# Optimization experiments

Hardware: AMD Instinct MI355X
Metric: run time of the kernel (lower is better)

## Reference

```python
import jax, jax.numpy as jnp
import numpy as np

# Sizes from init_kwargs / input_specs
D_MODEL = 1024; D_INT = 64; KW = 32; B = 2; L = 4096
SAMPLING = np.array([5, 5, 2, 1, 1]); DILATIONS = np.array([1, 1, 2, 4, 8])
SUBHEADS = len(SAMPLING); HEADS = int(SAMPLING.sum())  # 5, 14
HEAD_OF_SUB = np.repeat(np.arange(SUBHEADS), SAMPLING)  # subhead index for each head
HEAD_DIL = np.repeat(DILATIONS, SAMPLING)                # dilation for each head


def _win_idx(dil):
    # centered dilated band, clipped at sequence edges -> [L, KW]
    offs = (np.arange(KW) - KW // 2) * dil
    return np.clip(np.arange(L)[:, None] + offs[None, :], 0, L - 1)

SUB_IDX = jnp.asarray(np.stack([_win_idx(d) for d in DILATIONS]))  # [SUBHEADS, L, KW]
HEAD_IDX = jnp.asarray(np.stack([_win_idx(d) for d in HEAD_DIL]))  # [HEADS, L, KW]


def setup_inputs() -> dict:
    rng = jax.random.key(0)
    ks = jax.random.split(rng, 9)
    n = lambda i, sh, sc=1.0: jax.random.normal(ks[i], sh, dtype=jnp.float32) * sc
    return dict(
        query=n(0, (B, L, D_MODEL)),
        key=n(1, (B, L, D_MODEL)),
        value=n(2, (B, L, D_MODEL)),
        Wq=n(3, (SUBHEADS, D_MODEL, D_INT), 0.02),
        bq=jnp.zeros((SUBHEADS, D_INT), jnp.float32),
        Wk=n(4, (SUBHEADS, D_MODEL, D_INT), 0.02),
        bk=jnp.zeros((SUBHEADS, D_INT), jnp.float32),
        Wv=n(5, (HEADS, D_MODEL, D_INT), 0.02),
        bv=jnp.zeros((HEADS, D_INT), jnp.float32),
        Ws=n(6, (HEADS, KW, KW), 0.05) + jnp.eye(KW, dtype=jnp.float32)[None],
        bs=jnp.zeros((HEADS, KW), jnp.float32),
        Wc=n(7, (HEADS * D_INT, D_MODEL), 0.02),
        bc=jnp.zeros((D_MODEL,), jnp.float32),
    )


def reference(query, key, value, Wq, bq, Wk, bk, Wv, bv, Ws, bs, Wc, bc):
    # per-subhead query/key projections: [S, B, L, Di]
    q = jnp.einsum('bld,sdi->sbli', query, Wq) + bq[:, None, None, :]
    k = jnp.einsum('bld,sdi->sbli', key, Wk) + bk[:, None, None, :]
    # per-head value projection: [H, B, L, Di]
    v = jnp.einsum('bld,hdi->hbli', value, Wv) + bv[:, None, None, :]
    # dilated banded key windows per subhead: [S, B, L, KW, Di]
    kw = jax.vmap(lambda kh, ix: kh[:, ix], in_axes=(0, 0))(k, SUB_IDX)
    # banded scores [S, B, L, KW]
    scores = jnp.einsum('sbli,sblki->sblk', q, kw) / jnp.sqrt(jnp.float32(D_INT))
    # supersample: replicate each subhead's scores to its heads -> [H, B, L, KW]
    scores_h = scores[HEAD_OF_SUB]
    # per-head positional supersampling linear on the score window
    sampled = jnp.einsum('hblk,hkm->hblm', scores_h, Ws) + bs[:, None, None, :]
    attn = jax.nn.softmax(sampled, axis=-1)
    # dilated value windows per head: [H, B, L, KW, Di]
    vw = jax.vmap(lambda vh, ix: vh[:, ix], in_axes=(0, 0))(v, HEAD_IDX)
    out = jnp.einsum('hblk,hblki->hbli', attn, vw)  # [H, B, L, Di]
    out = jnp.transpose(out, (1, 2, 0, 3)).reshape(B, L, HEADS * D_INT)
    return out @ Wc + bc  # [B, L, D_MODEL]
```

## Files before the change

### kernel.cpp

```cpp
#include <hip/hip_runtime.h>
#include <math.h>

#define D_MODEL 1024
#define D_INT   64
#define KW      32
#define L_SEQ   4096
#define SUBHEADS 5
#define HEADS   14
#define M_ROWS  8192
#define N_CAT   896
#define NQK     320

typedef unsigned short us;
typedef unsigned int   uu;
typedef __attribute__((ext_vector_type(4))) unsigned int uu4;
typedef __attribute__((ext_vector_type(8))) short bf16x8_t;
typedef __attribute__((ext_vector_type(4))) float f32x4_t;

__device__ __forceinline__ float u2f(uu u) {
    float f; __builtin_memcpy(&f, &u, 4); return f;
}
__device__ __forceinline__ float blo(uu u) { return u2f(u << 16); }
__device__ __forceinline__ float bhi(uu u) { return u2f(u & 0xffff0000u); }
__device__ __forceinline__ us f2b(float f) {
    uu u; __builtin_memcpy(&u, &f, 4);
    u += 0x7fffu + ((u >> 16) & 1u);
    return (us)(u >> 16);
}
__device__ __forceinline__ uu pack2(float a, float b) {
    return (uu)f2b(a) | ((uu)f2b(b) << 16);
}
__device__ __forceinline__ uu cvtpk(float a, float b) {
    uu r;
    asm("v_cvt_pk_bf16_f32 %0, %1, %2" : "=v"(r) : "v"(a), "v"(b));
    return r;
}
__device__ __forceinline__ void load16(void* lds, const void* g) {
    __builtin_amdgcn_global_load_lds(
        (const __attribute__((address_space(1))) unsigned int*)g,
        (__attribute__((address_space(3))) unsigned int*)lds, 16, 0, 0);
}
__device__ __forceinline__ int subhead_of(int h) {
    return (h < 5) ? 0 : (h < 10) ? 1 : (h < 12) ? 2 : (h == 12) ? 3 : 4;
}
__device__ __forceinline__ int dil_of_sub(int s) {
    return (s <= 1) ? 1 : (1 << (s - 1));
}

__global__ __launch_bounds__(256)
void prep_kernel(const float* __restrict__ Wq, const float* __restrict__ Wk,
                 const float* __restrict__ Wv, const float* __restrict__ Wc,
                 us* __restrict__ Wqt, us* __restrict__ Wkt,
                 us* __restrict__ Wvt, us* __restrict__ Wct)
{
    __shared__ float t[32][33];
    const int tid = threadIdx.x;
    int g = blockIdx.x;
    const float* S; us* D; int K, N;
    if (g < 640) {
        if (g < 320) { S = Wq; D = Wqt; } else { S = Wk; D = Wkt; g -= 320; }
        K = 1024; N = 64;
    } else if (g < 1536) {
        g -= 640; S = Wv; D = Wvt; K = 1024; N = 64;
    } else {
        g -= 1536; S = Wc; D = Wct; K = 896; N = 1024;
    }
    const int nkx = K >> 5;
    const int kx = g % nkx;
    const int rest = g / nkx;
    const int ny = rest % (N >> 5);
    const int z  = rest / (N >> 5);
    const int k0 = kx * 32, n0 = ny * 32;
    S += (size_t)z * K * N;
    D += (size_t)z * K * N;
    const int tx = tid & 31, ty = tid >> 5;
#pragma unroll
    for (int r = 0; r < 32; r += 8)
        t[r + ty][tx] = S[(size_t)(k0 + r + ty) * N + n0 + tx];
    __syncthreads();
#pragma unroll
    for (int r = 0; r < 32; r += 8)
        D[(size_t)(n0 + r + ty) * K + k0 + tx] = f2b(t[tx][r + ty]);
}

template<bool AF32>
__device__ __forceinline__
void gemm64_core(const void* __restrict__ Av, const us* __restrict__ Bt,
                 const float* __restrict__ bias, us* __restrict__ C,
                 int K, int ldC, int row0, int col0, us* As, us* Bs)
{
    const int tid = threadIdx.x, w = tid >> 6, lane = tid & 63;
    const int m = lane & 15, quad = lane >> 4;
    const int sr = lane >> 3;
    const int scs = (lane & 7) ^ sr;

    f32x4_t z4 = {0.f, 0.f, 0.f, 0.f};
    f32x4_t acc[2][4] = {{z4, z4, z4, z4}, {z4, z4, z4, z4}};

    for (int k0 = 0; k0 < K; k0 += 64) {
#pragma unroll
        for (int p = 0; p < 2; p++) {
            const int r = w * 16 + p * 8 + sr;
            load16(&Bs[(w * 16 + p * 8) * 64], Bt + (size_t)(col0 + r) * K + k0 + scs * 8);
        }
#pragma unroll
        for (int p = 0; p < 4; p++) {
            const int r = w * 32 + p * 8 + sr;
            if constexpr (AF32) {
                const float* ag = (const float*)Av + (size_t)(row0 + r) * K + k0 + scs * 8;
                float4 x0 = *(const float4*)ag;
                float4 x1 = *(const float4*)(ag + 4);
                uu4 o;
                o.x = cvtpk(x0.x, x0.y); o.y = cvtpk(x0.z, x0.w);
                o.z = cvtpk(x1.x, x1.y); o.w = cvtpk(x1.z, x1.w);
                *(uu4*)&As[(w * 32 + p * 8 + sr) * 64 + (lane & 7) * 8] = o;
            } else {
                load16(&As[(w * 32 + p * 8) * 64],
                       (const us*)Av + (size_t)(row0 + r) * K + k0 + scs * 8);
            }
        }
        __syncthreads();
#pragma unroll
        for (int ks = 0; ks < 2; ks++) {
            const int slot = ((ks * 4 + quad) ^ (m & 7)) * 8;
            bf16x8_t a0 = *(const bf16x8_t*)&As[(w * 32 + m) * 64 + slot];
            bf16x8_t a1 = *(const bf16x8_t*)&As[(w * 32 + 16 + m) * 64 + slot];
#pragma unroll
            for (int t = 0; t < 4; t++) {
                bf16x8_t bb = *(const bf16x8_t*)&Bs[(t * 16 + m) * 64 + slot];
                acc[0][t] = __builtin_amdgcn_mfma_f32_16x16x32_bf16(a0, bb, acc[0][t], 0, 0, 0);
                acc[1][t] = __builtin_amdgcn_mfma_f32_16x16x32_bf16(a1, bb, acc[1][t], 0, 0, 0);
            }
        }
        __syncthreads();
    }

#pragma unroll
    for (int tm = 0; tm < 2; tm++) {
        const int rbase = row0 + w * 32 + tm * 16 + quad * 4;
#pragma unroll
        for (int t = 0; t < 4; t++) {
            const int col = col0 + t * 16 + m;
            const float bi = bias[col];
#pragma unroll
            for (int r = 0; r < 4; r++)
                C[(size_t)(rbase + r) * ldC + col] = f2b(acc[tm][t][r] + bi);
        }
    }
}

template<bool AF32>
__device__ __forceinline__
void gemm128_core(const void* __restrict__ Av, const us* __restrict__ Bt,
                  const float* __restrict__ bias, void* __restrict__ Cv,
                  int K, int ldC, int outBf16, int row0, int col0,
                  us* As, us* Bs)
{
    const int tid = threadIdx.x, w = tid >> 6, lane = tid & 63;
    const int m = lane & 15, quad = lane >> 4;
    const int sr = lane >> 3;
    const int scs = (lane & 7) ^ sr;
    const int mrow0 = (w & 1) * 64, ncol0 = (w >> 1) * 64;

    f32x4_t z = {0.f, 0.f, 0.f, 0.f};
    f32x4_t acc[4][4] = {{z,z,z,z},{z,z,z,z},{z,z,z,z},{z,z,z,z}};

    for (int k0 = 0; k0 < K; k0 += 64) {
#pragma unroll
        for (int p = 0; p < 4; p++) {
            const int r = w * 32 + p * 8 + sr;
            load16(&Bs[(w * 32 + p * 8) * 64], Bt + (size_t)(col0 + r) * K + k0 + scs * 8);
            if constexpr (AF32) {
                const float* ag = (const float*)Av + (size_t)(row0 + r) * K + k0 + scs * 8;
                float4 x0 = *(const float4*)ag;
                float4 x1 = *(const float4*)(ag + 4);
                uu4 o;
                o.x = cvtpk(x0.x, x0.y); o.y = cvtpk(x0.z, x0.w);
                o.z = cvtpk(x1.x, x1.y); o.w = cvtpk(x1.z, x1.w);
                *(uu4*)&As[(w * 32 + p * 8 + sr) * 64 + (lane & 7) * 8] = o;
            } else {
                load16(&As[(w * 32 + p * 8) * 64],
                       (const us*)Av + (size_t)(row0 + r) * K + k0 + scs * 8);
            }
        }
        __syncthreads();
#pragma unroll
        for (int ks = 0; ks < 2; ks++) {
            const int slot = ((ks * 4 + quad) ^ (m & 7)) * 8;
            bf16x8_t a[4], b[4];
#pragma unroll
            for (int t = 0; t < 4; t++) {
                a[t] = *(const bf16x8_t*)&As[(mrow0 + t * 16 + m) * 64 + slot];
                b[t] = *(const bf16x8_t*)&Bs[(ncol0 + t * 16 + m) * 64 + slot];
            }
#pragma unroll
            for (int i = 0; i < 4; i++)
#pragma unroll
                for (int j = 0; j < 4; j++)
                    acc[i][j] = __builtin_amdgcn_mfma_f32_16x16x32_bf16(a[i], b[j], acc[i][j], 0, 0, 0);
        }
        __syncthreads();
    }

#pragma unroll
    for (int i = 0; i < 4; i++) {
        const int rbase = row0 + mrow0 + i * 16 + quad * 4;
        if (outBf16) {
            us* Cb = (us*)Cv;
#pragma unroll
            for (int j = 0; j < 4; j++) {
                const int col = col0 + ncol0 + j * 16 + m;
                const float bi = bias[col];
#pragma unroll
                for (int r = 0; r < 4; r++)
                    Cb[(size_t)(rbase + r) * ldC + col] = f2b(acc[i][j][r] + bi);
            }
        } else {
            float* Cb = (float*)Cv;
#pragma unroll
            for (int j = 0; j < 4; j++) {
                const int col = col0 + ncol0 + j * 16 + m;
                const float bi = bias[col];
#pragma unroll
                for (int r = 0; r < 4; r++)
                    Cb[(size_t)(rbase + r) * ldC + col] = acc[i][j][r] + bi;
            }
        }
    }
}

__global__ __launch_bounds__(256)
void proj_kernel(const float* __restrict__ q, const float* __restrict__ k,
                 const float* __restrict__ v,
                 const us* __restrict__ Wqt, const us* __restrict__ Wkt,
                 const us* __restrict__ Wvt,
                 const float* __restrict__ bq, const float* __restrict__ bk,
                 const float* __restrict__ bv,
                 us* __restrict__ qbuf, us* __restrict__ kbuf,
                 us* __restrict__ vbuf)
{
    __shared__ us As[128 * 64];
    __shared__ us Bs[128 * 64];
    const int b = blockIdx.x;
    if (b < 448) {
        const int bx = b & 63, cy = b >> 6;
        gemm128_core<true>(v, Wvt, bv, vbuf, D_MODEL, N_CAT, 1,
                           bx << 7, cy << 7, As, Bs);
    } else {
        const int idx = b - 448;
        const int bx = idx & 63;
        const int rest = idx >> 6;
        const int cy = rest % 5, z = rest / 5;
        gemm64_core<true>(z ? (const void*)k : (const void*)q,
                          z ? Wkt : Wqt, z ? bk : bq,
                          z ? kbuf : qbuf, D_MODEL, NQK,
                          bx << 7, cy << 6, As, Bs);
    }
}

__global__ __launch_bounds__(256)
void gemm_out(const us* __restrict__ ab, const us* __restrict__ Wct,
              const float* __restrict__ bc, float* __restrict__ out)
{
    __shared__ us As[128 * 64];
    __shared__ us Bs[128 * 64];
    gemm128_core<false>(ab, Wct, bc, out, N_CAT, D_MODEL, 0,
                        (int)(blockIdx.x << 7), (int)(blockIdx.y << 7), As, Bs);
}

template<int ROWS>
__global__ __launch_bounds__(256)
void score_kernel(const us* __restrict__ qb, const us* __restrict__ kb,
                  float* __restrict__ scores, int sbase)
{
    __shared__ uu kslab[ROWS * 36];
    __shared__ uu qslab[64 * 32];

    const int tid  = threadIdx.x;
    const int wave = tid >> 6;
    const int lane = tid & 63;
    const int j    = lane & 31;
    const int half = lane >> 5;
    const int s    = sbase + blockIdx.y;
    const int d    = dil_of_sub(s);
    const int ml0  = blockIdx.x * 64;
    const int l0   = ml0 & 4095;
    const int bm   = ml0 - l0;
    const int W    = 64 + 31 * d;

    const uu* kg = (const uu*)kb;
    const uu* qg = (const uu*)qb;

    for (int idx = tid; idx < W * 32; idx += 256) {
        int r = idx >> 5, c = idx & 31;
        int src = l0 - 16 * d + r;
        src = src < 0 ? 0 : (src > 4095 ? 4095 : src);
        kslab[r * 36 + c] = kg[(size_t)(bm + src) * 160 + s * 32 + c];
    }
    for (int idx = tid; idx < 64 * 32; idx += 256) {
        int r = idx >> 5, c = idx & 31;
        qslab[r * 32 + c] = qg[(size_t)(ml0 + r) * 160 + s * 32 + c];
    }
    __syncthreads();

#pragma unroll
    for (int i = 0; i < 8; i++) {
        const int p = wave * 16 + i * 2 + half;
        const uu4* k4 = (const uu4*)&kslab[(p + j * d) * 36];
        const uu4* q4 = (const uu4*)&qslab[p * 32];
        float acc = 0.f;
#pragma unroll
        for (int q = 0; q < 8; q++) {
            uu4 kd = k4[q];
            uu4 qd = q4[q];
            acc = fmaf(blo(kd.x), blo(qd.x), acc); acc = fmaf(bhi(kd.x), bhi(qd.x), acc);
            acc = fmaf(blo(kd.y), blo(qd.y), acc); acc = fmaf(bhi(kd.y), bhi(qd.y), acc);
            acc = fmaf(blo(kd.z), blo(qd.z), acc); acc = fmaf(bhi(kd.z), bhi(qd.z), acc);
            acc = fmaf(blo(kd.w), blo(qd.w), acc); acc = fmaf(bhi(kd.w), bhi(qd.w), acc);
        }
        scores[((size_t)s * M_ROWS + ml0 + p) * 32 + j] = acc * 0.125f;
    }
}

template<int ROWS>
__global__ __launch_bounds__(256)
void head_kernel(const float* __restrict__ scores, const us* __restrict__ vb,
                 const float* __restrict__ Ws, const float* __restrict__ bs,
                 us* __restrict__ ab, int hbase)
{
    __shared__ uu    vslab[ROWS * 36];
    __shared__ float sab[64 * 36];

    const int tid  = threadIdx.x;
    const int wave = tid >> 6;
    const int lane = tid & 63;
    const int j    = lane & 31;
    const int half = lane >> 5;
    const int h    = hbase + blockIdx.y;
    const int s    = subhead_of(h);
    const int d    = dil_of_sub(s);
    const int ml0  = blockIdx.x * 64;
    const int l0   = ml0 & 4095;
    const int bm   = ml0 - l0;
    const int W    = 64 + 31 * d;

    const uu* vg = (const uu*)vb;
    for (int idx = tid; idx < W * 32; idx += 256) {
        int r = idx >> 5, c = idx & 31;
        int src = l0 - 16 * d + r;
        src = src < 0 ? 0 : (src > 4095 ? 4095 : src);
        vslab[r * 36 + c] = vg[(size_t)(bm + src) * 448 + h * 32 + c];
    }
    {
        const float4* g4 = (const float4*)(scores + ((size_t)s * M_ROWS + ml0) * 32);
#pragma unroll
        for (int t = 0; t < 2; t++) {
            int i4 = t * 256 + tid;
            int r = i4 >> 3, c4 = i4 & 7;
            *(float4*)&sab[r * 36 + c4 * 4] = g4[i4];
        }
    }
    float wsr[32];
#pragma unroll
    for (int k = 0; k < 32; k++) wsr[k] = Ws[(size_t)h * 1024 + k * 32 + j];
    const float bsv = bs[h * 32 + j];
    __syncthreads();

#pragma unroll
    for (int i = 0; i < 8; i++) {
        const int p = wave * 16 + i * 2 + half;
        const float4* s4 = (const float4*)&sab[p * 36];
        float acc = bsv;
#pragma unroll
        for (int q = 0; q < 8; q++) {
            float4 v = s4[q];
            acc = fmaf(v.x, wsr[q * 4 + 0], acc);
            acc = fmaf(v.y, wsr[q * 4 + 1], acc);
            acc = fmaf(v.z, wsr[q * 4 + 2], acc);
            acc = fmaf(v.w, wsr[q * 4 + 3], acc);
        }
        float mx = acc;
#pragma unroll
        for (int off = 16; off > 0; off >>= 1) mx = fmaxf(mx, __shfl_xor(mx, off, 64));
        float ex = __expf(acc - mx);
        float sum = ex;
#pragma unroll
        for (int off = 16; off > 0; off >>= 1) sum += __shfl_xor(sum, off, 64);
        sab[p * 36 + j] = ex / sum;
    }

    const int o = lane >> 3;
    const int c = lane & 7;
#pragma unroll
    for (int pass = 0; pass < 2; pass++) {
        const int p  = wave * 16 + pass * 8 + o;
        const int ml = ml0 + p;
        float a0 = 0.f, a1 = 0.f, a2 = 0.f, a3 = 0.f;
        float a4 = 0.f, a5 = 0.f, a6 = 0.f, a7 = 0.f;
#pragma unroll
        for (int mm = 0; mm < 32; mm++) {
            const float at = sab[p * 36 + mm];
            uu4 vd = *(const uu4*)&vslab[(p + mm * d) * 36 + c * 4];
            a0 = fmaf(blo(vd.x), at, a0); a1 = fmaf(bhi(vd.x), at, a1);
            a2 = fmaf(blo(vd.y), at, a2); a3 = fmaf(bhi(vd.y), at, a3);
            a4 = fmaf(blo(vd.z), at, a4); a5 = fmaf(bhi(vd.z), at, a5);
            a6 = fmaf(blo(vd.w), at, a6); a7 = fmaf(bhi(vd.w), at, a7);
        }
        uu4 od;
        od.x = pack2(a0, a1); od.y = pack2(a2, a3);
        od.z = pack2(a4, a5); od.w = pack2(a6, a7);
        *(uu4*)&((uu*)ab)[(size_t)ml * 448 + h * 32 + c * 4] = od;
    }
}

extern "C" void kernel_launch(void* const* d_in, const int* in_sizes, int n_in,
                              void* d_out, int out_size, void* d_ws, size_t ws_size,
                              hipStream_t stream)
{
    const float* query = (const float*)d_in[0];
    const float* key   = (const float*)d_in[1];
    const float* value = (const float*)d_in[2];
    const float* Wq    = (const float*)d_in[3];
    const float* bq    = (const float*)d_in[4];
    const float* Wk    = (const float*)d_in[5];
    const float* bk    = (const float*)d_in[6];
    const float* Wv    = (const float*)d_in[7];
    const float* bv    = (const float*)d_in[8];
    const float* Ws    = (const float*)d_in[9];
    const float* bs    = (const float*)d_in[10];
    const float* Wc    = (const float*)d_in[11];
    const float* bc    = (const float*)d_in[12];
    float* out = (float*)d_out;

    us* w = (us*)d_ws;
    us* Xq  = w;
    us* ab  = w;
    us* Xk  = Xq  + (size_t)M_ROWS * D_MODEL;
    float* scores = (float*)Xk;
    us* Xv  = Xk  + (size_t)M_ROWS * D_MODEL;
    us* Wqt = Xv  + (size_t)M_ROWS * D_MODEL;
    us* Wkt = Wqt + (size_t)SUBHEADS * D_INT * D_MODEL;
    us* Wvt = Wkt + (size_t)SUBHEADS * D_INT * D_MODEL;
    us* Wct = Wvt + (size_t)HEADS * D_INT * D_MODEL;
    us* qbuf = Wct + (size_t)D_MODEL * N_CAT;
    us* kbuf = qbuf + (size_t)M_ROWS * NQK;
    us* vbuf = kbuf + (size_t)M_ROWS * NQK;

    dim3 blk(256);

    prep_kernel<<<dim3(2432), blk, 0, stream>>>(
        Wq, Wk, Wv, Wc, Wqt, Wkt, Wvt, Wct);

    proj_kernel<<<dim3(1088), blk, 0, stream>>>(
        query, key, value, Wqt, Wkt, Wvt, bq, bk, bv, qbuf, kbuf, vbuf);

    score_kernel<126><<<dim3(M_ROWS / 64, 3), blk, 0, stream>>>(qbuf, kbuf, scores, 0);
    score_kernel<312><<<dim3(M_ROWS / 64, 2), blk, 0, stream>>>(qbuf, kbuf, scores, 3);

    head_kernel<312><<<dim3(M_ROWS / 64, 2),  blk, 0, stream>>>(scores, vbuf, Ws, bs, ab, 12);
    head_kernel<126><<<dim3(M_ROWS / 64, 12), blk, 0, stream>>>(scores, vbuf, Ws, bs, ab, 0);

    gemm_out<<<dim3(M_ROWS / 128, D_MODEL / 128), blk, 0, stream>>>(
        ab, Wct, bc, out);
}
```

Baseline: 288.7 us.

## Prefetch next fp32 A tile into registers during MFMA compute in GEMM cores

Both GEMM cores now load the first K-tile before the loop. For the fp32 A path, each iteration issues the next tile's global loads into registers before the MFMA block, then converts and stores them to LDS after a barrier. The bf16 and B-tile loads still happen after compute, behind the barrier. The aim is to hide global load latency of the fp32 activations behind MFMA work, at the cost of extra registers that may lower occupancy.

```diff
diff --git a/kernel.cpp b/kernel.cpp
--- a/kernel.cpp
+++ b/kernel.cpp
@@ -97,29 +97,49 @@
     f32x4_t z4 = {0.f, 0.f, 0.f, 0.f};
     f32x4_t acc[2][4] = {{z4, z4, z4, z4}, {z4, z4, z4, z4}};
 
+    float4 pa[4][2];
+
+#pragma unroll
+    for (int p = 0; p < 2; p++) {
+        const int r = w * 16 + p * 8 + sr;
+        load16(&Bs[(w * 16 + p * 8) * 64], Bt + (size_t)(col0 + r) * K + scs * 8);
+    }
+#pragma unroll
+    for (int p = 0; p < 4; p++) {
+        const int r = w * 32 + p * 8 + sr;
+        if constexpr (AF32) {
+            const float* ag = (const float*)Av + (size_t)(row0 + r) * K + scs * 8;
+            pa[p][0] = *(const float4*)ag;
+            pa[p][1] = *(const float4*)(ag + 4);
+        } else {
+            load16(&As[(w * 32 + p * 8) * 64],
+                   (const us*)Av + (size_t)(row0 + r) * K + scs * 8);
+        }
+    }
+    if constexpr (AF32) {
+#pragma unroll
+        for (int p = 0; p < 4; p++) {
+            uu4 o;
+            o.x = cvtpk(pa[p][0].x, pa[p][0].y); o.y = cvtpk(pa[p][0].z, pa[p][0].w);
+            o.z = cvtpk(pa[p][1].x, pa[p][1].y); o.w = cvtpk(pa[p][1].z, pa[p][1].w);
+            *(uu4*)&As[(w * 32 + p * 8 + sr) * 64 + (lane & 7) * 8] = o;
+        }
+    }
+    __syncthreads();
+
     for (int k0 = 0; k0 < K; k0 += 64) {
-#pragma unroll
-        for (int p = 0; p < 2; p++) {
-            const int r = w * 16 + p * 8 + sr;
-            load16(&Bs[(w * 16 + p * 8) * 64], Bt + (size_t)(col0 + r) * K + k0 + scs * 8);
-        }
-#pragma unroll
-        for (int p = 0; p < 4; p++) {
-            const int r = w * 32 + p * 8 + sr;
-            if constexpr (AF32) {
-                const float* ag = (const float*)Av + (size_t)(row0 + r) * K + k0 + scs * 8;
-                float4 x0 = *(const float4*)ag;
-                float4 x1 = *(const float4*)(ag + 4);
-                uu4 o;
-                o.x = cvtpk(x0.x, x0.y); o.y = cvtpk(x0.z, x0.w);
-                o.z = cvtpk(x1.x, x1.y); o.w = cvtpk(x1.z, x1.w);
-                *(uu4*)&As[(w * 32 + p * 8 + sr) * 64 + (lane & 7) * 8] = o;
-            } else {
-                load16(&As[(w * 32 + p * 8) * 64],
-                       (const us*)Av + (size_t)(row0 + r) * K + k0 + scs * 8);
-            }
-        }
-        __syncthreads();
+        const int kn = k0 + 64;
+        if constexpr (AF32) {
+            if (kn < K) {
+#pragma unroll
+                for (int p = 0; p < 4; p++) {
+                    const int r = w * 32 + p * 8 + sr;
+                    const float* ag = (const float*)Av + (size_t)(row0 + r) * K + kn + scs * 8;
+                    pa[p][0] = *(const float4*)ag;
+                    pa[p][1] = *(const float4*)(ag + 4);
+                }
+            }
+        }
 #pragma unroll
         for (int ks = 0; ks < 2; ks++) {
             const int slot = ((ks * 4 + quad) ^ (m & 7)) * 8;
@@ -132,7 +152,31 @@
                 acc[1][t] = __builtin_amdgcn_mfma_f32_16x16x32_bf16(a1, bb, acc[1][t], 0, 0, 0);
             }
         }
-        __syncthreads();
+        if (kn < K) {
+            __builtin_amdgcn_s_barrier();
+#pragma unroll
+            for (int p = 0; p < 2; p++) {
+                const int r = w * 16 + p * 8 + sr;
+                load16(&Bs[(w * 16 + p * 8) * 64], Bt + (size_t)(col0 + r) * K + kn + scs * 8);
+            }
+            if constexpr (AF32) {
+#pragma unroll
+                for (int p = 0; p < 4; p++) {
+                    uu4 o;
+                    o.x = cvtpk(pa[p][0].x, pa[p][0].y); o.y = cvtpk(pa[p][0].z, pa[p][0].w);
+                    o.z = cvtpk(pa[p][1].x, pa[p][1].y); o.w = cvtpk(pa[p][1].z, pa[p][1].w);
+                    *(uu4*)&As[(w * 32 + p * 8 + sr) * 64 + (lane & 7) * 8] = o;
+                }
+            } else {
+#pragma unroll
+                for (int p = 0; p < 4; p++) {
+                    const int r = w * 32 + p * 8 + sr;
+                    load16(&As[(w * 32 + p * 8) * 64],
+                           (const us*)Av + (size_t)(row0 + r) * K + kn + scs * 8);
+                }
+            }
+            __syncthreads();
+        }
     }
 
 #pragma unroll
@@ -165,25 +209,45 @@
     f32x4_t z = {0.f, 0.f, 0.f, 0.f};
     f32x4_t acc[4][4] = {{z,z,z,z},{z,z,z,z},{z,z,z,z},{z,z,z,z}};
 
+    float4 pa[4][2];
+
+#pragma unroll
+    for (int p = 0; p < 4; p++) {
+        const int r = w * 32 + p * 8 + sr;
+        load16(&Bs[(w * 32 + p * 8) * 64], Bt + (size_t)(col0 + r) * K + scs * 8);
+        if constexpr (AF32) {
+            const float* ag = (const float*)Av + (size_t)(row0 + r) * K + scs * 8;
+            pa[p][0] = *(const float4*)ag;
+            pa[p][1] = *(const float4*)(ag + 4);
+        } else {
+            load16(&As[(w * 32 + p * 8) * 64],
+                   (const us*)Av + (size_t)(row0 + r) * K + scs * 8);
+        }
+    }
+    if constexpr (AF32) {
+#pragma unroll
+        for (int p = 0; p < 4; p++) {
+            uu4 o;
+            o.x = cvtpk(pa[p][0].x, pa[p][0].y); o.y = cvtpk(pa[p][0].z, pa[p][0].w);
+            o.z = cvtpk(pa[p][1].x, pa[p][1].y); o.w = cvtpk(pa[p][1].z, pa[p][1].w);
+            *(uu4*)&As[(w * 32 + p * 8 + sr) * 64 + (lane & 7) * 8] = o;
+        }
+    }
+    __syncthreads();
+
     for (int k0 = 0; k0 < K; k0 += 64) {
-#pragma unroll
-        for (int p = 0; p < 4; p++) {
-            const int r = w * 32 + p * 8 + sr;
-            load16(&Bs[(w * 32 + p * 8) * 64], Bt + (size_t)(col0 + r) * K + k0 + scs * 8);
-            if constexpr (AF32) {
-                const float* ag = (const float*)Av + (size_t)(row0 + r) * K + k0 + scs * 8;
-                float4 x0 = *(const float4*)ag;
-                float4 x1 = *(const float4*)(ag + 4);
-                uu4 o;
-                o.x = cvtpk(x0.x, x0.y); o.y = cvtpk(x0.z, x0.w);
-                o.z = cvtpk(x1.x, x1.y); o.w = cvtpk(x1.z, x1.w);
-                *(uu4*)&As[(w * 32 + p * 8 + sr) * 64 + (lane & 7) * 8] = o;
-            } else {
-                load16(&As[(w * 32 + p * 8) * 64],
-                       (const us*)Av + (size_t)(row0 + r) * K + k0 + scs * 8);
-            }
-        }
-        __syncthreads();
+        const int kn = k0 + 64;
+        if constexpr (AF32) {
+            if (kn < K) {
+#pragma unroll
+                for (int p = 0; p < 4; p++) {
+                    const int r = w * 32 + p * 8 + sr;
+                    const float* ag = (const float*)Av + (size_t)(row0 + r) * K + kn + scs * 8;
+                    pa[p][0] = *(const float4*)ag;
+                    pa[p][1] = *(const float4*)(ag + 4);
+                }
+            }
+        }
 #pragma unroll
         for (int ks = 0; ks < 2; ks++) {
             const int slot = ((ks * 4 + quad) ^ (m & 7)) * 8;
@@ -199,7 +263,28 @@
                 for (int j = 0; j < 4; j++)
                     acc[i][j] = __builtin_amdgcn_mfma_f32_16x16x32_bf16(a[i], b[j], acc[i][j], 0, 0, 0);
         }
-        __syncthreads();
+        if (kn < K) {
+            __builtin_amdgcn_s_barrier();
+#pragma unroll
+            for (int p = 0; p < 4; p++) {
+                const int r = w * 32 + p * 8 + sr;
+                load16(&Bs[(w * 32 + p * 8) * 64], Bt + (size_t)(col0 + r) * K + kn + scs * 8);
+                if constexpr (!AF32) {
+                    load16(&As[(w * 32 + p * 8) * 64],
+                           (const us*)Av + (size_t)(row0 + r) * K + kn + scs * 8);
+                }
+            }
+            if constexpr (AF32) {
+#pragma unroll
+                for (int p = 0; p < 4; p++) {
+                    uu4 o;
+                    o.x = cvtpk(pa[p][0].x, pa[p][0].y); o.y = cvtpk(pa[p][0].z, pa[p][0].w);
+                    o.z = cvtpk(pa[p][1].x, pa[p][1].y); o.w = cvtpk(pa[p][1].z, pa[p][1].w);
+                    *(uu4*)&As[(w * 32 + p * 8 + sr) * 64 + (lane & 7) * 8] = o;
+                }
+            }
+            __syncthreads();
+        }
     }
 
 #pragma unroll
```

After: 286.2 us. Within noise of the previous version (-0.9%).
